# Kernel optimization log

Measured on AMD Instinct MI355X. Metric: run time of the kernel, lower is better.

Reference implementation:

```python
import jax, jax.numpy as jnp
import numpy as np

K = 16  # centroids per codebook (4-bit LUT indices, blink-mm convention)


def _im2col(x, kh, kw, stride, pad):
    # x: [B, C, H, W] -> [B, P, C*kh*kw] with channel-major feature ordering
    # (each length-(kh*kw) subvector is one channel's patch, matching the
    #  per-channel codebook layout of the 3x3 AMM conv).
    B, C, H, W = x.shape
    xp = jnp.pad(x, ((0, 0), (0, 0), (pad, pad), (pad, pad)))
    Ho = (H + 2 * pad - kh) // stride + 1
    Wo = (W + 2 * pad - kw) // stride + 1
    cols = [xp[:, :, i:i + stride * Ho:stride, j:j + stride * Wo:stride]
            for i in range(kh) for j in range(kw)]  # fixed small loop (<=9)
    feat = jnp.stack(cols, axis=2)                      # [B, C, kh*kw, Ho, Wo]
    feat = feat.reshape(B, C * kh * kw, Ho, Wo)
    feat = feat.transpose(0, 2, 3, 1).reshape(B, Ho * Wo, C * kh * kw)
    return feat, Ho, Wo


def _amm_conv_bn_act(x, centroids, lut, scale, bias, kernel, stride, pad, relu):
    # Product-quantization approximate matmul conv:
    #  1) im2col, split feature dim D into ncodebooks subspaces of dim dsub
    #  2) nearest-centroid (L2) assignment per subspace -> 4-bit index
    #  3) gather+accumulate precomputed LUT dot products over codebooks
    #  4) folded BatchNorm affine + optional ReLU
    feat, Ho, Wo = _im2col(x, kernel, kernel, stride, pad)
    B, P, D = feat.shape
    ncb, k, dsub = centroids.shape
    xs = feat.reshape(B, P, ncb, dsub)
    dots = jnp.einsum('bpcd,ckd->bpck', xs, centroids)          # [B,P,ncb,K]
    c2 = jnp.sum(centroids * centroids, axis=-1)                # [ncb,K]
    idx = jnp.argmin(c2[None, None] - 2.0 * dots, axis=-1)      # [B,P,ncb]
    onehot = jax.nn.one_hot(idx, k, dtype=x.dtype)              # [B,P,ncb,K]
    out = jnp.einsum('bpck,cko->bpo', onehot, lut)              # LUT accumulate
    out = out * scale + bias                                    # folded BN
    if relu:
        out = jax.nn.relu(out)
    Cout = lut.shape[-1]
    return out.reshape(B, Ho, Wo, Cout).transpose(0, 3, 1, 2)


def setup_inputs() -> dict:
    key = jax.random.key(0)
    ks = jax.random.split(key, 16)
    inplanes, planes, width = 1024, 256, 256
    B, H, W = 32, 14, 14
    d = {}
    d['x'] = jax.random.normal(ks[0], (B, inplanes, H, W), dtype=jnp.float32)
    d['c1_centroids'] = jax.random.normal(ks[1], (inplanes // 4, K, 4), dtype=jnp.float32)
    d['c1_lut'] = jax.random.normal(ks[2], (inplanes // 4, K, width), dtype=jnp.float32) * 0.1
    d['c1_scale'] = jax.random.uniform(ks[3], (width,), dtype=jnp.float32, minval=0.5, maxval=1.5)
    d['c1_bias'] = jax.random.normal(ks[4], (width,), dtype=jnp.float32) * 0.1
    d['c2_centroids'] = jax.random.normal(ks[5], (width, K, 9), dtype=jnp.float32)
    d['c2_lut'] = jax.random.normal(ks[6], (width, K, width), dtype=jnp.float32) * 0.1
    d['c2_scale'] = jax.random.uniform(ks[7], (width,), dtype=jnp.float32, minval=0.5, maxval=1.5)
    d['c2_bias'] = jax.random.normal(ks[8], (width,), dtype=jnp.float32) * 0.1
    d['c3_centroids'] = jax.random.normal(ks[9], (width // 4, K, 4), dtype=jnp.float32)
    d['c3_lut'] = jax.random.normal(ks[10], (width // 4, K, planes * 4), dtype=jnp.float32) * 0.1
    d['c3_scale'] = jax.random.uniform(ks[11], (planes * 4,), dtype=jnp.float32, minval=0.5, maxval=1.5)
    d['c3_bias'] = jax.random.normal(ks[12], (planes * 4,), dtype=jnp.float32) * 0.1
    return d


def reference(x, c1_centroids, c1_lut, c1_scale, c1_bias,
              c2_centroids, c2_lut, c2_scale, c2_bias,
              c3_centroids, c3_lut, c3_scale, c3_bias):
    identity = x
    out = _amm_conv_bn_act(x, c1_centroids, c1_lut, c1_scale, c1_bias,
                           kernel=1, stride=1, pad=0, relu=True)
    out = _amm_conv_bn_act(out, c2_centroids, c2_lut, c2_scale, c2_bias,
                           kernel=3, stride=1, pad=1, relu=True)
    out = _amm_conv_bn_act(out, c3_centroids, c3_lut, c3_scale, c3_bias,
                           kernel=1, stride=1, pad=0, relu=False)
    # QuantizedAdd + QuantizedReLU (float reference math: add then relu)
    return jax.nn.relu(out + identity)
```

## Files before the change

kernel.cpp:

```cpp
#include <hip/hip_runtime.h>
#include <stdint.h>

#define PP 196
#define BP 6272

typedef _Float16 half_t;
typedef half_t half8v __attribute__((ext_vector_type(8)));
typedef half_t half2v __attribute__((ext_vector_type(2)));


template <typename T>
__global__ __launch_bounds__(256) void assign_1x1(
    const T* __restrict__ in, const float* __restrict__ cents,
    uint32_t* __restrict__ idxp, int nchan) {
  __shared__ float  sf[8][16][4];
  __shared__ double sd[8][16][6];
  const int chunk = blockIdx.y;
  const int t = threadIdx.x;
  for (int i = t; i < 512; i += 256) {
    float c = cents[(size_t)chunk * 512 + i];
    int cb = i >> 6, r = i & 63;
    sf[cb][r >> 2][r & 3] = c;
    sd[cb][r >> 2][1 + (r & 3)] = (double)c;
  }
  __syncthreads();
  if (t < 128) {
    int cb = t >> 4, k = t & 15;
    double s = 0.0;
#pragma unroll
    for (int d = 0; d < 4; d++) { double c = sd[cb][k][1 + d]; s += c * c; }
    sd[cb][k][0] = s;
  }
  __syncthreads();
  const int p = blockIdx.x * 256 + t;
  if (p >= BP) return;
  const unsigned b = (unsigned)p / 196u;
  const unsigned pr = (unsigned)p - b * 196u;
  const T* xb = in + ((size_t)b * nchan + chunk * 32) * PP + pr;
  T xr[32];
#pragma unroll
  for (int i = 0; i < 32; i++) xr[i] = xb[(size_t)i * PP];
  float xs2[32];
#pragma unroll
  for (int i = 0; i < 32; i++) xs2[i] = 2.f * (float)xr[i];
  uint32_t word = 0;
#pragma unroll 1
  for (int cb = 0; cb < 8; cb++) {
    float best = 1e30f, sec = 1e30f; int bi = 0;
#pragma unroll
    for (int k = 0; k < 16; k++) {
      const float4 c = *(const float4*)&sf[cb][k][0];
      float dist = c.x * (c.x - xs2[cb * 4 + 0]);
      dist = fmaf(c.y, c.y - xs2[cb * 4 + 1], dist);
      dist = fmaf(c.z, c.z - xs2[cb * 4 + 2], dist);
      dist = fmaf(c.w, c.w - xs2[cb * 4 + 3], dist);
      if (dist < best) { sec = best; best = dist; bi = k; }
      else sec = fminf(sec, dist);
    }
    if (__any(sec - best < 2e-4f)) {
      double xv[4];
#pragma unroll
      for (int d = 0; d < 4; d++) xv[d] = (double)xr[cb * 4 + d];
      double bb = 1e300; int bi64 = 0;
#pragma unroll
      for (int k = 0; k < 16; k++) {
        double dot = 0.0;
#pragma unroll
        for (int d = 0; d < 4; d++) dot = fma(xv[d], sd[cb][k][1 + d], dot);
        double dist = sd[cb][k][0] - 2.0 * dot;
        if (dist < bb) { bb = dist; bi64 = k; }
      }
      bi = bi64;
    }
    word |= (uint32_t)bi << (4 * cb);
  }
  idxp[(size_t)chunk * BP + p] = word;
}

__global__ __launch_bounds__(256) void assign_3x3(
    const double* __restrict__ in, const float* __restrict__ cents,
    uint32_t* __restrict__ idxp) {
  __shared__ float  sf[8][16][12];
  __shared__ double sd[8][16][10];
  const int chunk = blockIdx.y;
  const int c0g = chunk * 8;
  const int t = threadIdx.x;
  for (int i = t; i < 1152; i += 256) {
    int cb = i / 144, r = i - cb * 144;
    int k = r / 9, d = r - k * 9;
    float c = cents[(size_t)(c0g + cb) * 144 + k * 9 + d];
    sf[cb][k][1 + d] = c;
    sd[cb][k][1 + d] = (double)c;
  }
  __syncthreads();
  if (t < 128) {
    int cb = t >> 4, k = t & 15;
    double s = 0.0;
    float s32 = 0.f;
#pragma unroll
    for (int d = 0; d < 9; d++) {
      double c = sd[cb][k][1 + d]; s += c * c;
      float cf = sf[cb][k][1 + d]; s32 += cf * cf;
    }
    sd[cb][k][0] = s;
    sf[cb][k][0] = s32;
  }
  __syncthreads();
  const int p = blockIdx.x * 256 + t;
  if (p >= BP) return;
  const unsigned b = (unsigned)p / 196u;
  const unsigned pr = (unsigned)p - b * 196u;
  const int oh = pr / 14, ow = pr - oh * 14;
  uint32_t word = 0;
#pragma unroll 1
  for (int cb = 0; cb < 8; cb++) {
    const double* base = in + ((size_t)b * 256 + (c0g + cb)) * PP;
    double v64[9]; float v32[9];
#pragma unroll
    for (int r = 0; r < 3; r++) {
#pragma unroll
      for (int cc = 0; cc < 3; cc++) {
        int hh = oh + r - 1, ww = ow + cc - 1;
        bool ok = (hh >= 0) & (hh < 14) & (ww >= 0) & (ww < 14);
        double v = ok ? base[hh * 14 + ww] : 0.0;
        v64[r * 3 + cc] = v;
        v32[r * 3 + cc] = (float)v;
      }
    }
    float best = 1e30f, sec = 1e30f; int bi = 0;
#pragma unroll
    for (int k = 0; k < 16; k++) {
      const float4 cA = *(const float4*)&sf[cb][k][0];
      const float4 cB = *(const float4*)&sf[cb][k][4];
      const float4 cC = *(const float4*)&sf[cb][k][8];
      float dot = v32[0] * cA.y;
      dot = fmaf(v32[1], cA.z, dot);
      dot = fmaf(v32[2], cA.w, dot);
      dot = fmaf(v32[3], cB.x, dot);
      dot = fmaf(v32[4], cB.y, dot);
      dot = fmaf(v32[5], cB.z, dot);
      dot = fmaf(v32[6], cB.w, dot);
      dot = fmaf(v32[7], cC.x, dot);
      dot = fmaf(v32[8], cC.y, dot);
      float dist = fmaf(-2.f, dot, cA.x);
      if (dist < best) { sec = best; best = dist; bi = k; }
      else sec = fminf(sec, dist);
    }
    if (__any(sec - best < 4e-4f)) {
      double bb = 1e300; int bi64 = 0;
#pragma unroll
      for (int k = 0; k < 16; k++) {
        double dot = 0.0;
#pragma unroll
        for (int d = 0; d < 9; d++) dot = fma(v64[d], sd[cb][k][1 + d], dot);
        double dist = sd[cb][k][0] - 2.0 * dot;
        if (dist < bb) { bb = dist; bi64 = k; }
      }
      bi = bi64;
    }
    word |= (uint32_t)bi << (4 * cb);
  }
  idxp[(size_t)chunk * BP + p] = word;
}

template <int NCB, int NOUT, bool RELU, bool FUSE3, typename OutT>
__global__ __launch_bounds__(256) void accum_f64(
    const float* __restrict__ lut, const uint32_t* __restrict__ idxp,
    const float* __restrict__ scale, const float* __restrict__ bias,
    const float* __restrict__ c3cent, uint8_t* __restrict__ i3b,
    OutT* __restrict__ out) {
  __shared__ float s_lut[16 * 16 * 20];
  __shared__ float  c3f[4][16][4];
  __shared__ float  c3c2f[4][16];
  __shared__ double c3d[4][16][4];
  __shared__ double c3c2d[4][16];
  const int t = threadIdx.x;
  const int lane = t & 63;
  const int q = t >> 6;
  const int p = blockIdx.x * 64 + lane;
  const int o_base = blockIdx.y * 16;
  if (FUSE3 && t < 64) {
    int cb_l = t >> 4, k = t & 15;
    const float4 cf = *(const float4*)(c3cent + ((size_t)(blockIdx.y * 4 + cb_l)) * 64 + k * 4);
    c3f[cb_l][k][0] = cf.x; c3f[cb_l][k][1] = cf.y;
    c3f[cb_l][k][2] = cf.z; c3f[cb_l][k][3] = cf.w;
    double d0 = (double)cf.x, d1 = (double)cf.y, d2 = (double)cf.z, d3 = (double)cf.w;
    c3d[cb_l][k][0] = d0; c3d[cb_l][k][1] = d1;
    c3d[cb_l][k][2] = d2; c3d[cb_l][k][3] = d3;
    double s = 0.0; s += d0 * d0; s += d1 * d1; s += d2 * d2; s += d3 * d3;
    c3c2d[cb_l][k] = s;
    float s32 = 0.f; s32 += cf.x * cf.x; s32 += cf.y * cf.y;
    s32 += cf.z * cf.z; s32 += cf.w * cf.w;
    c3c2f[cb_l][k] = s32;
  }
  const int srow = t >> 2, scol = t & 3;
  const float* src = lut + (size_t)srow * NOUT + o_base + scol * 4;
  const int d0f = srow * 20 + scol * 4;
  double a0 = 0, a1 = 0, a2 = 0, a3 = 0;
  constexpr int NCHUNK = NCB / 16;
  for (int ch = 0; ch < NCHUNK; ch++) {
    __syncthreads();
    uint32_t w0 = idxp[(size_t)(ch * 2) * BP + p];
    uint32_t w1 = idxp[(size_t)(ch * 2 + 1) * BP + p];
    {
      const float* g = src + (size_t)(ch * 256) * NOUT;
#pragma unroll
      for (int j = 0; j < 4; j++) {
        float4 v = *(const float4*)(g + (size_t)(64 * j) * NOUT);
        *(float4*)(s_lut + d0f + j * 1280) = v;
      }
    }
    __syncthreads();
#pragma unroll
    for (int j = 0; j < 8; j++) {
      uint32_t w = (j < 4) ? w0 : w1;
      int sh = (j & 3) * 8;
      int i0 = (int)((w >> sh) & 15u);
      int i1 = (int)((w >> (sh + 4)) & 15u);
      const float4 va = *(const float4*)(s_lut + (2 * j) * 320 + i0 * 20 + q * 4);
      const float4 vb = *(const float4*)(s_lut + (2 * j + 1) * 320 + i1 * 20 + q * 4);
      float s0 = va.x + vb.x, s1 = va.y + vb.y;
      float s2 = va.z + vb.z, s3 = va.w + vb.w;
      a0 += (double)s0; a1 += (double)s1; a2 += (double)s2; a3 += (double)s3;
    }
  }
  const unsigned b = (unsigned)p / 196u;
  const unsigned pr = (unsigned)p - b * 196u;
  const int o = o_base + q * 4;
  const float4 sc = *(const float4*)(scale + o);
  const float4 bs = *(const float4*)(bias + o);
  double r0 = a0 * (double)sc.x + (double)bs.x;
  double r1 = a1 * (double)sc.y + (double)bs.y;
  double r2 = a2 * (double)sc.z + (double)bs.z;
  double r3 = a3 * (double)sc.w + (double)bs.w;
  if (RELU) {
    r0 = fmax(r0, 0.0); r1 = fmax(r1, 0.0);
    r2 = fmax(r2, 0.0); r3 = fmax(r3, 0.0);
  }
  if (FUSE3) {
    const int cb_l = q;
    float x0 = (float)r0, x1 = (float)r1, x2 = (float)r2, x3 = (float)r3;
    float best = 1e30f, sec = 1e30f; int bi = 0;
#pragma unroll
    for (int k = 0; k < 16; k++) {
      const float4 c = *(const float4*)&c3f[cb_l][k][0];
      float dot = x0 * c.x;
      dot = fmaf(x1, c.y, dot);
      dot = fmaf(x2, c.z, dot);
      dot = fmaf(x3, c.w, dot);
      float dist = fmaf(-2.f, dot, c3c2f[cb_l][k]);
      if (dist < best) { sec = best; best = dist; bi = k; }
      else sec = fminf(sec, dist);
    }
    if (__any(sec - best < 1e-3f)) {
      double bb = 1e300; int bi64 = 0;
#pragma unroll
      for (int k = 0; k < 16; k++) {
        double dot = 0.0;
        dot = fma(r0, c3d[cb_l][k][0], dot);
        dot = fma(r1, c3d[cb_l][k][1], dot);
        dot = fma(r2, c3d[cb_l][k][2], dot);
        dot = fma(r3, c3d[cb_l][k][3], dot);
        double dist = c3c2d[cb_l][k] - 2.0 * dot;
        if (dist < bb) { bb = dist; bi64 = k; }
      }
      bi = bi64;
    }
    i3b[(size_t)p * 64 + blockIdx.y * 4 + q] = (uint8_t)bi;
  } else {
    OutT* op = out + ((size_t)b * NOUT + o) * PP + pr;
    op[0 * PP] = (OutT)r0; op[1 * PP] = (OutT)r1;
    op[2 * PP] = (OutT)r2; op[3 * PP] = (OutT)r3;
  }
}

__global__ __launch_bounds__(256) void accum3_f16(
    const float* __restrict__ lut, const uint8_t* __restrict__ i3b,
    const float* __restrict__ scale, const float* __restrict__ bias,
    const float* __restrict__ res, float* __restrict__ out) {
  __shared__ half_t s16[16 * 640];
  const int t = threadIdx.x;
  const int lane = t & 63;
  const int wave = t >> 6;
  const int h = wave & 1;
  const int pg = wave >> 1;
  const int p = blockIdx.x * 128 + pg * 64 + lane;
  const int o_base = blockIdx.y * 16;
  const int s0 = t, s1 = t + 256;
  const int cA = s0 >> 5, kA = (s0 >> 1) & 15, hA = s0 & 1;
  const int cB = s1 >> 5, kB = (s1 >> 1) & 15, hB = s1 & 1;
  const size_t cs = (size_t)16 * 16 * 1024;
  constexpr int NCHUNK = 4;
  float acc[8];
#pragma unroll
  for (int i = 0; i < 8; i++) acc[i] = 0.f;
  for (int ch = 0; ch < NCHUNK; ch++) {
    __syncthreads();
    const uint4 iw = *(const uint4*)(i3b + (size_t)p * 64 + ch * 16);
    {
      const float* gA = lut + (size_t)ch * cs + ((size_t)cA * 16 + kA) * 1024 + o_base + hA * 8;
      const float* gB = lut + (size_t)ch * cs + ((size_t)cB * 16 + kB) * 1024 + o_base + hB * 8;
      float4 a0 = *(const float4*)gA;
      float4 a1 = *(const float4*)(gA + 4);
      float4 b0 = *(const float4*)gB;
      float4 b1 = *(const float4*)(gB + 4);
      half8v va, vb;
      va[0] = (half_t)a0.x; va[1] = (half_t)a0.y; va[2] = (half_t)a0.z; va[3] = (half_t)a0.w;
      va[4] = (half_t)a1.x; va[5] = (half_t)a1.y; va[6] = (half_t)a1.z; va[7] = (half_t)a1.w;
      vb[0] = (half_t)b0.x; vb[1] = (half_t)b0.y; vb[2] = (half_t)b0.z; vb[3] = (half_t)b0.w;
      vb[4] = (half_t)b1.x; vb[5] = (half_t)b1.y; vb[6] = (half_t)b1.z; vb[7] = (half_t)b1.w;
      *(half8v*)(s16 + cA * 640 + kA * 40 + hA * 8) = va;
      *(half8v*)(s16 + cB * 640 + kB * 40 + hB * 8) = vb;
    }
    __syncthreads();
#pragma unroll
    for (int grp = 0; grp < 2; grp++) {
      uint32_t wa = grp ? iw.z : iw.x;
      uint32_t wb = grp ? iw.w : iw.y;
      half2v p0 = 0, p1 = 0, p2 = 0, p3 = 0;
#pragma unroll
      for (int j = 0; j < 8; j++) {
        uint32_t w = (j < 4) ? wa : wb;
        int idx = (int)((w >> ((j & 3) * 8)) & 15u);
        int cb_l = grp * 8 + j;
        const half8v v = *(const half8v*)(s16 + cb_l * 640 + idx * 40 + h * 8);
        const half2v* vp = (const half2v*)&v;
        p0 += vp[0]; p1 += vp[1]; p2 += vp[2]; p3 += vp[3];
      }
      acc[0] += (float)p0[0]; acc[1] += (float)p0[1];
      acc[2] += (float)p1[0]; acc[3] += (float)p1[1];
      acc[4] += (float)p2[0]; acc[5] += (float)p2[1];
      acc[6] += (float)p3[0]; acc[7] += (float)p3[1];
    }
  }
  const unsigned b = (unsigned)p / 196u;
  const unsigned pr = (unsigned)p - b * 196u;
  const int o = o_base + h * 8;
  const float* rp = res + ((size_t)b * 1024 + o) * PP + pr;
  float* op = out + ((size_t)b * 1024 + o) * PP + pr;
#pragma unroll
  for (int i = 0; i < 8; i++) {
    float v = acc[i] * scale[o + i] + bias[o + i] + rp[(size_t)i * PP];
    op[(size_t)i * PP] = fmaxf(v, 0.f);
  }
}


extern "C" void kernel_launch(void* const* d_in, const int* in_sizes, int n_in,
                              void* d_out, int out_size, void* d_ws, size_t ws_size,
                              hipStream_t stream) {
  const float* x   = (const float*)d_in[0];
  const float* c1c = (const float*)d_in[1];
  const float* c1l = (const float*)d_in[2];
  const float* c1s = (const float*)d_in[3];
  const float* c1b = (const float*)d_in[4];
  const float* c2c = (const float*)d_in[5];
  const float* c2l = (const float*)d_in[6];
  const float* c2s = (const float*)d_in[7];
  const float* c2b = (const float*)d_in[8];
  const float* c3c = (const float*)d_in[9];
  const float* c3l = (const float*)d_in[10];
  const float* c3s = (const float*)d_in[11];
  const float* c3b = (const float*)d_in[12];

  const size_t sz_i1  = (size_t)32 * BP * 4;
  const size_t sz_i2  = (size_t)32 * BP * 4;
  const size_t sz_i3b = (size_t)BP * 64;
  const size_t sz_o64 = (size_t)BP * 256 * 8;

  char* w = (char*)d_ws;
  uint32_t* i1 = (uint32_t*)w; w += sz_i1;
  uint32_t* i2 = (uint32_t*)w; w += sz_i2;
  uint8_t* i3b = (uint8_t*)w;  w += sz_i3b;
  double* out1;
  if (ws_size >= (size_t)(w - (char*)d_ws) + sz_o64) {
    out1 = (double*)w;
  } else {
    out1 = (double*)d_out;
  }

  const dim3 blkA(256), blkC(256);
  assign_1x1<float><<<dim3(25, 32), blkA, 0, stream>>>(x, c1c, i1, 1024);
  accum_f64<256, 256, true, false, double><<<dim3(98, 16), blkC, 0, stream>>>(
      c1l, i1, c1s, c1b, nullptr, nullptr, out1);
  assign_3x3<<<dim3(25, 32), blkA, 0, stream>>>(out1, c2c, i2);
  accum_f64<256, 256, true, true, double><<<dim3(98, 16), blkC, 0, stream>>>(
      c2l, i2, c2s, c2b, c3c, i3b, nullptr);
  accum3_f16<<<dim3(49, 64), blkC, 0, stream>>>(
      c3l, i3b, c3s, c3b, x, (float*)d_out);
}
```

Measured before the change: 235.6 us.

## Double-buffer LUT staging in accum kernel with direct global-to-LDS async loads

Replaces the synchronous per-chunk LUT copy through registers with global_load_lds DMA into a double-buffered shared array. The next chunk's LUT is prefetched while the current one is gathered. Chunks shrink from 16 to 8 codebooks and the LDS layout drops its padding. This aims to hide global load latency and avoid register round-trips, at the cost of manual waitcnt and barrier handling that is fragile and may cause LDS bank conflicts without the padding.

```diff
diff --git a/kernel.cpp b/kernel.cpp
--- a/kernel.cpp
+++ b/kernel.cpp
@@ -7,6 +7,12 @@
 typedef _Float16 half_t;
 typedef half_t half8v __attribute__((ext_vector_type(8)));
 typedef half_t half2v __attribute__((ext_vector_type(2)));
+
+__device__ __forceinline__ void dma16(const float* g, float* l) {
+  __builtin_amdgcn_global_load_lds(
+      (const __attribute__((address_space(1))) float*)g,
+      (__attribute__((address_space(3))) float*)l, 16, 0, 0);
+}
 
 
 template <typename T>
@@ -169,7 +175,7 @@
     const float* __restrict__ scale, const float* __restrict__ bias,
     const float* __restrict__ c3cent, uint8_t* __restrict__ i3b,
     OutT* __restrict__ out) {
-  __shared__ float s_lut[16 * 16 * 20];
+  __shared__ float s_lut[2 * 2048];
   __shared__ float  c3f[4][16][4];
   __shared__ float  c3c2f[4][16];
   __shared__ double c3d[4][16][4];
@@ -193,36 +199,46 @@
     s32 += cf.z * cf.z; s32 += cf.w * cf.w;
     c3c2f[cb_l][k] = s32;
   }
-  const int srow = t >> 2, scol = t & 3;
-  const float* src = lut + (size_t)srow * NOUT + o_base + scol * 4;
-  const int d0f = srow * 20 + scol * 4;
+  __syncthreads();
+
+  const float* src0 = lut + ((size_t)(t >> 6) * 16 + (t & 15)) * NOUT
+                          + o_base + ((t >> 4) & 3) * 4;
+  float* dst0 = s_lut + (t >> 6) * 256;
+  constexpr int NCHUNK = NCB / 8;
+  constexpr size_t CSTRIDE = (size_t)128 * NOUT;
   double a0 = 0, a1 = 0, a2 = 0, a3 = 0;
-  constexpr int NCHUNK = NCB / 16;
+  dma16(src0, dst0);
+  dma16(src0 + 64 * NOUT, dst0 + 1024);
+#pragma unroll 1
   for (int ch = 0; ch < NCHUNK; ch++) {
-    __syncthreads();
-    uint32_t w0 = idxp[(size_t)(ch * 2) * BP + p];
-    uint32_t w1 = idxp[(size_t)(ch * 2 + 1) * BP + p];
-    {
-      const float* g = src + (size_t)(ch * 256) * NOUT;
-#pragma unroll
-      for (int j = 0; j < 4; j++) {
-        float4 v = *(const float4*)(g + (size_t)(64 * j) * NOUT);
-        *(float4*)(s_lut + d0f + j * 1280) = v;
-      }
-    }
-    __syncthreads();
-#pragma unroll
-    for (int j = 0; j < 8; j++) {
-      uint32_t w = (j < 4) ? w0 : w1;
-      int sh = (j & 3) * 8;
-      int i0 = (int)((w >> sh) & 15u);
-      int i1 = (int)((w >> (sh + 4)) & 15u);
-      const float4 va = *(const float4*)(s_lut + (2 * j) * 320 + i0 * 20 + q * 4);
-      const float4 vb = *(const float4*)(s_lut + (2 * j + 1) * 320 + i1 * 20 + q * 4);
+    const uint32_t w = idxp[(size_t)ch * BP + p];
+    __builtin_amdgcn_sched_barrier(0);
+    if (ch + 1 < NCHUNK) {
+      const float* s = src0 + (size_t)(ch + 1) * CSTRIDE;
+      float* d = dst0 + ((ch + 1) & 1) * 2048;
+      dma16(s, d);
+      dma16(s + 64 * NOUT, d + 1024);
+      __builtin_amdgcn_sched_barrier(0);
+      asm volatile("s_waitcnt vmcnt(2)" ::: "memory");
+    } else {
+      asm volatile("s_waitcnt vmcnt(0)" ::: "memory");
+    }
+    __builtin_amdgcn_sched_barrier(0);
+    __builtin_amdgcn_s_barrier();
+    __builtin_amdgcn_sched_barrier(0);
+    const float* buf = s_lut + (ch & 1) * 2048 + q * 64;
+#pragma unroll
+    for (int j = 0; j < 4; j++) {
+      int i0 = (int)((w >> (8 * j)) & 15u);
+      int i1 = (int)((w >> (8 * j + 4)) & 15u);
+      const float4 va = *(const float4*)(buf + (2 * j) * 256 + i0 * 4);
+      const float4 vb = *(const float4*)(buf + (2 * j + 1) * 256 + i1 * 4);
       float s0 = va.x + vb.x, s1 = va.y + vb.y;
       float s2 = va.z + vb.z, s3 = va.w + vb.w;
       a0 += (double)s0; a1 += (double)s1; a2 += (double)s2; a3 += (double)s3;
     }
+    __builtin_amdgcn_sched_barrier(0);
+    __builtin_amdgcn_s_barrier();
   }
   const unsigned b = (unsigned)p / 196u;
   const unsigned pr = (unsigned)p - b * 196u;
```

After: 277.6 us. 1.18x slower.

## Double-buffer LUT tiles in shared memory with register prefetch in accum kernel

Applied to the files above, without the earlier changes.

Moves the LUT staging in the accumulate kernel to a double-buffered shared-memory scheme. The tile for chunk ch+2 is prefetched into registers while chunk ch+1 is written to the alternate buffer, and the index words are prefetched one chunk ahead. This cuts the loop from two barriers per chunk to one and hides global load latency behind the gather-accumulate work. The shared layout also changes from a padded row-of-20 layout to a per-output-quad layout, which alters LDS bank access patterns and doubles LDS use, possibly lowering occupancy.

```diff
diff --git a/kernel.cpp b/kernel.cpp
--- a/kernel.cpp
+++ b/kernel.cpp
@@ -169,7 +169,7 @@
     const float* __restrict__ scale, const float* __restrict__ bias,
     const float* __restrict__ c3cent, uint8_t* __restrict__ i3b,
     OutT* __restrict__ out) {
-  __shared__ float s_lut[16 * 16 * 20];
+  __shared__ float s_lut[2 * 4096];
   __shared__ float  c3f[4][16][4];
   __shared__ float  c3c2f[4][16];
   __shared__ double c3d[4][16][4];
@@ -193,36 +193,59 @@
     s32 += cf.z * cf.z; s32 += cf.w * cf.w;
     c3c2f[cb_l][k] = s32;
   }
-  const int srow = t >> 2, scol = t & 3;
-  const float* src = lut + (size_t)srow * NOUT + o_base + scol * 4;
-  const int d0f = srow * 20 + scol * 4;
+
+  const float* src0 = lut + ((size_t)(t >> 6) * 16 + (t & 15)) * NOUT
+                          + o_base + ((t >> 4) & 3) * 4;
+  constexpr int NCHUNK = NCB / 16;
+  constexpr size_t CSTRIDE = (size_t)256 * NOUT;
+  float4 rj[4];
+#pragma unroll
+  for (int j = 0; j < 4; j++)
+    rj[j] = *(const float4*)(src0 + (size_t)(64 * j) * NOUT);
+#pragma unroll
+  for (int j = 0; j < 4; j++)
+    *(float4*)(s_lut + (t + 256 * j) * 4) = rj[j];
+#pragma unroll
+  for (int j = 0; j < 4; j++)
+    rj[j] = *(const float4*)(src0 + CSTRIDE + (size_t)(64 * j) * NOUT);
+  uint32_t w0 = idxp[p];
+  uint32_t w1 = idxp[(size_t)BP + p];
+  __syncthreads();
+
   double a0 = 0, a1 = 0, a2 = 0, a3 = 0;
-  constexpr int NCHUNK = NCB / 16;
+#pragma unroll 1
   for (int ch = 0; ch < NCHUNK; ch++) {
-    __syncthreads();
-    uint32_t w0 = idxp[(size_t)(ch * 2) * BP + p];
-    uint32_t w1 = idxp[(size_t)(ch * 2 + 1) * BP + p];
-    {
-      const float* g = src + (size_t)(ch * 256) * NOUT;
-#pragma unroll
-      for (int j = 0; j < 4; j++) {
-        float4 v = *(const float4*)(g + (size_t)(64 * j) * NOUT);
-        *(float4*)(s_lut + d0f + j * 1280) = v;
-      }
-    }
-    __syncthreads();
+    const uint32_t cw0 = w0, cw1 = w1;
+    if (ch + 1 < NCHUNK) {
+      float* d = s_lut + ((ch + 1) & 1) * 4096;
+#pragma unroll
+      for (int j = 0; j < 4; j++)
+        *(float4*)(d + (t + 256 * j) * 4) = rj[j];
+    }
+    if (ch + 2 < NCHUNK) {
+      const float* s = src0 + (size_t)(ch + 2) * CSTRIDE;
+#pragma unroll
+      for (int j = 0; j < 4; j++)
+        rj[j] = *(const float4*)(s + (size_t)(64 * j) * NOUT);
+    }
+    if (ch + 1 < NCHUNK) {
+      w0 = idxp[(size_t)(2 * ch + 2) * BP + p];
+      w1 = idxp[(size_t)(2 * ch + 3) * BP + p];
+    }
+    const float* buf = s_lut + (ch & 1) * 4096 + q * 64;
 #pragma unroll
     for (int j = 0; j < 8; j++) {
-      uint32_t w = (j < 4) ? w0 : w1;
+      uint32_t w = (j < 4) ? cw0 : cw1;
       int sh = (j & 3) * 8;
       int i0 = (int)((w >> sh) & 15u);
       int i1 = (int)((w >> (sh + 4)) & 15u);
-      const float4 va = *(const float4*)(s_lut + (2 * j) * 320 + i0 * 20 + q * 4);
-      const float4 vb = *(const float4*)(s_lut + (2 * j + 1) * 320 + i1 * 20 + q * 4);
+      const float4 va = *(const float4*)(buf + (2 * j) * 256 + i0 * 4);
+      const float4 vb = *(const float4*)(buf + (2 * j + 1) * 256 + i1 * 4);
       float s0 = va.x + vb.x, s1 = va.y + vb.y;
       float s2 = va.z + vb.z, s3 = va.w + vb.w;
       a0 += (double)s0; a1 += (double)s1; a2 += (double)s2; a3 += (double)s3;
     }
+    __syncthreads();
   }
   const unsigned b = (unsigned)p / 196u;
   const unsigned pr = (unsigned)p - b * 196u;
```

Result: slower. 422.8 us (+79.5%).
